# Optimization experiments

Hardware: AMD Instinct MI355X
Metric: run time of the kernel (lower is better)

Reference implementation:

```python
import jax, jax.numpy as jnp
import numpy as np

V, E, H, L, T, B, S = 50000, 256, 512, 2, 22, 64, 512
HH = H // 2
START, STOP = T - 2, T - 1  # START_TAG, STOP_TAG appended to tagset


def _lstm_cell(x, h, c, wih, whh, b):
    # PyTorch gate order: i, f, g, o
    g = x @ wih.T + h @ whh.T + b
    i, f, gg, o = jnp.split(g, 4, axis=-1)
    c2 = jax.nn.sigmoid(f) * c + jax.nn.sigmoid(i) * jnp.tanh(gg)
    h2 = jax.nn.sigmoid(o) * jnp.tanh(c2)
    return h2, c2


def _run_dir(xs, ms, h0, c0, wih, whh, b, reverse):
    # xs: [S,B,E], ms: [S,B] bool. Packed-sequence semantics: no state update
    # and zero (pad-value) output at padded steps.
    def step(carry, inp):
        h, c = carry
        xt, mt = inp
        h2, c2 = _lstm_cell(xt, h, c, wih, whh, b)
        m = mt[:, None]
        h = jnp.where(m, h2, h)
        c = jnp.where(m, c2, c)
        return (h, c), jnp.where(m, h, 0.0)
    _, outs = jax.lax.scan(step, (h0, c0), (xs, ms), reverse=reverse)
    return outs


def _forward_feats(sentence, lengths, emb, wih_f, whh_f, b_f, wih_b, whh_b, b_b,
                   h1_0, c1_0, wih_s, whh_s, b_s, h2_0, c2_0, W_tag, b_tag):
    Bq, Sq = sentence.shape
    x = emb[sentence]                                       # [B,S,E]
    ms = (jnp.arange(Sq)[None, :] < lengths[:, None]).T     # [S,B]
    xs = jnp.transpose(x, (1, 0, 2))                        # [S,B,E]
    bc = lambda p: jnp.broadcast_to(p, (Bq, p.shape[-1]))
    out_f = _run_dir(xs, ms, bc(h1_0[0]), bc(c1_0[0]), wih_f, whh_f, b_f, False)
    out_b = _run_dir(xs, ms, bc(h1_0[1]), bc(c1_0[1]), wih_b, whh_b, b_b, True)
    bi = jnp.concatenate([out_f, out_b], axis=-1)           # [S,B,H]

    h0 = jnp.broadcast_to(h2_0, (L, Bq, H))
    c0 = jnp.broadcast_to(c2_0, (L, Bq, H))

    def step(carry, xt):
        h, c = carry
        inp = xt
        hs, cs = [], []
        for l in range(L):  # small fixed layer count
            h2, c2 = _lstm_cell(inp, h[l], c[l], wih_s[l], whh_s[l], b_s[l])
            inp = h2
            hs.append(h2)
            cs.append(c2)
        return (jnp.stack(hs), jnp.stack(cs)), inp

    _, outs = jax.lax.scan(step, (h0, c0), bi)              # [S,B,H]
    feats = jnp.einsum('sbh,th->sbt', outs, W_tag) + b_tag  # [S,B,T]
    return feats, ms


def _viterbi(feats, ms, trans):
    # trans[i, j] = score of transitioning from tag j to tag i
    Tn = trans.shape[0]
    score = feats[0] + trans[:, START][None, :]             # [B,T]

    def vstep(score, inp):
        ft, mt = inp
        cand = score[:, None, :] + trans[None, :, :]        # [B, to, from]
        ns = jnp.max(cand, axis=2) + ft
        bp = jnp.argmax(cand, axis=2)
        m = mt[:, None]
        score = jnp.where(m, ns, score)
        bp = jnp.where(m, bp, jnp.arange(Tn)[None, :])      # identity at pad
        return score, bp

    score, bps = jax.lax.scan(vstep, score, (feats[1:], ms[1:]))
    terminal = score + trans[STOP][None, :]
    best_score = jnp.max(terminal, axis=1)                  # [B]
    best_tag = jnp.argmax(terminal, axis=1)                 # [B]

    def bt(tag, bp):
        nt = jnp.take_along_axis(bp, tag[:, None], axis=1)[:, 0]
        return nt, nt

    _, rest = jax.lax.scan(bt, best_tag, bps, reverse=True)  # [S-1,B]
    tags = jnp.concatenate([rest, best_tag[None, :]], axis=0).T  # [B,S]
    return best_score, tags


def setup_inputs() -> dict:
    key = jax.random.key(0)
    ks = iter(jax.random.split(key, 24))
    sc = 0.08
    n = lambda shape: jax.random.normal(next(ks), shape, dtype=jnp.float32) * sc
    return dict(
        sentence=jax.random.randint(next(ks), (B, S), 0, V),
        lengths=jax.random.randint(next(ks), (B,), 1, S + 1),
        emb=n((V, E)),
        wih_f=n((4 * HH, E)), whh_f=n((4 * HH, HH)), b_f=n((4 * HH,)),
        wih_b=n((4 * HH, E)), whh_b=n((4 * HH, HH)), b_b=n((4 * HH,)),
        h1_0=n((2, 1, HH)), c1_0=n((2, 1, HH)),
        wih_s=n((L, 4 * H, H)), whh_s=n((L, 4 * H, H)), b_s=n((L, 4 * H)),
        h2_0=n((L, 1, H)), c2_0=n((L, 1, H)),
        W_tag=n((T, H)), b_tag=n((T,)),
        trans=n((T, T)),
    )


def reference(sentence, lengths, emb, wih_f, whh_f, b_f, wih_b, whh_b, b_b,
              h1_0, c1_0, wih_s, whh_s, b_s, h2_0, c2_0, W_tag, b_tag, trans):
    feats, ms = _forward_feats(sentence, lengths, emb, wih_f, whh_f, b_f,
                               wih_b, whh_b, b_b, h1_0, c1_0,
                               wih_s, whh_s, b_s, h2_0, c2_0, W_tag, b_tag)
    score, tag_seq = _viterbi(feats, ms, trans)
    return score, tag_seq
```

## Files before the change

### kernel.cpp

```cpp
#include <hip/hip_runtime.h>
#include <cmath>


namespace {
constexpr int SS = 512;
constexpr int BB = 64;
constexpr int EE = 256;
constexpr int HHd = 256;
constexpr int HD = 512;
constexpr int NTAG = 22;
constexpr int TSTART = 20;
constexpr int TSTOP = 21;

constexpr size_t OFF_BI    = 0;
constexpr size_t OFF_H1H   = OFF_BI    + (size_t)SS * HD * BB;
constexpr size_t OFF_XT    = OFF_H1H   + (size_t)(SS + 1) * HD * BB;
constexpr size_t OFF_FEATS = OFF_XT    + (size_t)SS * EE * BB;
constexpr size_t OFF_H0R   = OFF_FEATS + (size_t)SS * NTAG * BB;
constexpr size_t OFF_HF    = OFF_H0R   + 2 * (size_t)HD * BB;
constexpr size_t OFF_HB    = OFF_HF    + 2 * (size_t)HHd * BB;
constexpr size_t OFF_BAR   = OFF_HB    + 2 * (size_t)HHd * BB;
constexpr int BAR_INTS = 1152;

constexpr size_t OFF_C0 = OFF_XT;
constexpr size_t OFF_C1 = OFF_XT + (size_t)HD * BB;
}

__device__ __forceinline__ int cidx(int k, int lane) {
  return ((k >> 2) << 8) + (lane << 2) + (k & 3);
}

__device__ __forceinline__ float4 cload4(const float4* p) {
  float4 r;
  asm volatile("global_load_dwordx4 %0, %1, off sc0 sc1" : "=v"(r) : "v"(p));
  return r;
}
__device__ __forceinline__ void vwait0() {
  asm volatile("s_waitcnt vmcnt(0)" ::: "memory");
}
__device__ __forceinline__ void cstore(float* p, float v) {
  __hip_atomic_store(p, v, __ATOMIC_RELAXED, __HIP_MEMORY_SCOPE_AGENT);
}

template <int NBLK>
__device__ __forceinline__ void gbarC(int* flags, int* release, int bid, int epoch) {
  __syncthreads();
  if (threadIdx.x == 0) {
    __hip_atomic_store(flags + bid, epoch + 1, __ATOMIC_RELAXED, __HIP_MEMORY_SCOPE_AGENT);
  }
  if (bid == 0) {
    if (threadIdx.x < 64) {
      constexpr int PER = NBLK / 64;
      bool ok;
      do {
        ok = true;
#pragma unroll
        for (int i = 0; i < PER; ++i) {
          ok = ok && (__hip_atomic_load(flags + threadIdx.x * PER + i, __ATOMIC_RELAXED,
                                        __HIP_MEMORY_SCOPE_AGENT) > epoch);
        }
      } while (__any(!ok));
      if (threadIdx.x == 0) {
        __hip_atomic_store(release, epoch + 1, __ATOMIC_RELAXED, __HIP_MEMORY_SCOPE_AGENT);
      }
    }
  } else {
    if (threadIdx.x == 0) {
      while (__hip_atomic_load(release, __ATOMIC_RELAXED, __HIP_MEMORY_SCOPE_AGENT) <= epoch) {
        __builtin_amdgcn_s_sleep(1);
      }
    }
  }
  __syncthreads();
}

__device__ __forceinline__ float sigm(float x) { return 1.f / (1.f + expf(-x)); }
__device__ __forceinline__ float comp4(float4 v, int w) {
  return (w == 0) ? v.x : (w == 1) ? v.y : (w == 2) ? v.z : v.w;
}

__global__ __launch_bounds__(256) void k0(const int* __restrict__ sent,
                                          const float* __restrict__ emb,
                                          float* __restrict__ xT) {
  const int t = blockIdx.x;
  const int lane = threadIdx.x & 63;
  const int w = __builtin_amdgcn_readfirstlane(threadIdx.x >> 6);
  __shared__ float tile[64][65];
  __shared__ int rows[64];
  if (threadIdx.x < 64) rows[threadIdx.x] = sent[(size_t)threadIdx.x * SS + t];
  __syncthreads();
  float4* xT4 = (float4*)xT;
  for (int e0 = 0; e0 < EE; e0 += 64) {
    for (int bb = 0; bb < 16; ++bb) {
      int b = bb * 4 + w;
      tile[b][lane] = emb[(size_t)rows[b] * EE + e0 + lane];
    }
    __syncthreads();
    for (int r = 0; r < 4; ++r) {
      int ecl = w * 4 + r;
      int ec = (e0 >> 2) + ecl;
      float4 v = make_float4(tile[lane][ecl * 4 + 0], tile[lane][ecl * 4 + 1],
                             tile[lane][ecl * 4 + 2], tile[lane][ecl * 4 + 3]);
      xT4[((size_t)t * 64 + ec) * 64 + lane] = v;
    }
    __syncthreads();
  }
}

struct K2A {
  const float* xT; float* bi;
  const float* wih_f; const float* whh_f; const float* b_f;
  const float* wih_b; const float* whh_b; const float* b_b;
  const float* h10; const float* c10; const int* lengths;
  float* hf; float* hb;
  int* bar;
};

__global__ __launch_bounds__(1024, 1) void k2(K2A a) {
  const int lane = threadIdx.x & 63;
  const int w = __builtin_amdgcn_readfirstlane((int)threadIdx.x >> 6);
  const int d = (int)blockIdx.x >> 7;
  const int lb = (int)blockIdx.x & 127;
  int* flags = a.bar + d * 384;
  int* release = a.bar + d * 384 + 160;
  const int u0 = lb * 2;
  const float* wih = d ? a.wih_b : a.wih_f;
  const float* whh = d ? a.whh_b : a.whh_f;
  const float* bias = d ? a.b_b : a.b_f;
  float* hbuf = d ? a.hb : a.hf;

  __shared__ float lw[8 * 512];
  __shared__ float4 part[16][2][64];

  {
    int f4 = (int)threadIdx.x;
    int r = f4 >> 7;
    int kk = (f4 & 127) * 4;
    int g = r >> 1, ul = r & 1;
    int grow = g * HHd + u0 + ul;
    float4 v = (kk < 256) ? *(const float4*)(wih + (size_t)grow * 256 + kk)
                          : *(const float4*)(whh + (size_t)grow * 256 + (kk - 256));
    *(float4*)(lw + r * 512 + kk) = v;
  }

  const int len = a.lengths[lane];
  float c_st = 0.f, h_old = 0.f;
  if (w < 2) {
    int u = u0 + w;
    h_old = a.h10[d * 256 + u];
    c_st = a.c10[d * 256 + u];
    cstore(&hbuf[cidx(u, lane)], h_old);
    vwait0();
  }
  int ep = 0;
  gbarC<128>(flags, release, lb, ep); ep++;

  const int ks = w * 32;
  const bool hpart = (w >= 8);
  const float4* lw4 = (const float4*)lw;
  int buf = 0;
  for (int step = 0; step < SS; ++step) {
    const int t = d ? (SS - 1 - step) : step;
    const float* actbase = hpart ? (hbuf + (size_t)buf * (HHd * 64))
                                 : (a.xT + (size_t)t * (EE * 64));
    const int ksl = hpart ? (ks - 256) : ks;
    const float4* p = (const float4*)actbase + (size_t)(ksl >> 2) * 64 + lane;
    float4 va[8];
    if (hpart) {
#pragma unroll
      for (int c = 0; c < 8; ++c) va[c] = cload4(p + (size_t)c * 64);
      vwait0();
    } else {
#pragma unroll
      for (int c = 0; c < 8; ++c) va[c] = p[(size_t)c * 64];
    }
    float acc[8] = {0, 0, 0, 0, 0, 0, 0, 0};
#pragma unroll
    for (int c = 0; c < 8; ++c) {
      float4 h = va[c];
#pragma unroll
      for (int r = 0; r < 8; ++r) {
        float4 wv = lw4[r * 128 + (ks >> 2) + c];
        acc[r] = fmaf(h.x, wv.x, acc[r]);
        acc[r] = fmaf(h.y, wv.y, acc[r]);
        acc[r] = fmaf(h.z, wv.z, acc[r]);
        acc[r] = fmaf(h.w, wv.w, acc[r]);
      }
    }
    part[w][0][lane] = make_float4(acc[0], acc[1], acc[2], acc[3]);
    part[w][1][lane] = make_float4(acc[4], acc[5], acc[6], acc[7]);
    __syncthreads();
    if (w < 2) {
      float qi = 0.f, qf = 0.f, qg = 0.f, qo = 0.f;
#pragma unroll
      for (int wv = 0; wv < 16; ++wv) {
        float4 p0 = part[wv][0][lane], p1 = part[wv][1][lane];
        qi += comp4(p0, w);  qf += comp4(p0, 2 + w);
        qg += comp4(p1, w);  qo += comp4(p1, 2 + w);
      }
      const int u = u0 + w;
      float gi = qi + bias[u];
      float gf = qf + bias[256 + u];
      float gg = qg + bias[512 + u];
      float go = qo + bias[768 + u];
      float i_ = sigm(gi), f_ = sigm(gf), o_ = sigm(go);
      float gn = tanhf(gg);
      float c2 = f_ * c_st + i_ * gn;
      float h2 = o_ * tanhf(c2);
      const bool m = (t < len);
      h2 = m ? h2 : h_old;
      c_st = m ? c2 : c_st;
      h_old = h2;
      cstore(&hbuf[(size_t)(buf ^ 1) * (HHd * 64) + cidx(u, lane)], h2);
      a.bi[(size_t)t * (HD * 64) + cidx(d * 256 + u, lane)] = m ? h2 : 0.f;
      vwait0();
    }
    buf ^= 1;
    gbarC<128>(flags, release, lb, ep); ep++;
  }
}

__global__ __launch_bounds__(512) void k4i(const float* __restrict__ h20,
                                           const float* __restrict__ c20,
                                           float* __restrict__ h0r,
                                           float* __restrict__ h1h,
                                           float* __restrict__ c0,
                                           float* __restrict__ c1) {
  const int layer = blockIdx.x;
  const int u = threadIdx.x;
  const float hv = h20[layer * 512 + u];
  const float cv = c20[layer * 512 + u];
  float* hd = layer ? h1h : h0r;
  float* cd = layer ? c1 : c0;
#pragma unroll 4
  for (int lane = 0; lane < 64; ++lane) {
    hd[cidx(u, lane)] = hv;
    cd[cidx(u, lane)] = cv;
  }
}

struct K4S {
  const float* bi; float* h0r; float* h1h;
  const float* wihs; const float* whhs; const float* bs;
  float* c0; float* c1;
};

__global__ __launch_bounds__(1024, 1) void k4s(K4S a, int t) {
  const int layer = (int)blockIdx.x >> 7;
  if (layer == 0) { if (t >= SS) return; } else { if (t < 1) return; }
  const int lane = threadIdx.x & 63;
  const int w = __builtin_amdgcn_readfirstlane((int)threadIdx.x >> 6);
  const int lb = (int)blockIdx.x & 127;
  const int u0 = lb * 4;
  const float* wih = a.wihs + (size_t)layer * (2048 * 512);
  const float* whh = a.whhs + (size_t)layer * (2048 * 512);

  __shared__ float part[8][16][64];

  float* cst = layer ? a.c1 : a.c0;
  float c_st = 0.f;
  if (w < 4) c_st = cst[cidx(u0 + w, lane)];

  const int ks = (w & 7) * 64;
  const bool hpart = (w >= 8);
  const float* wsel = hpart ? whh : wih;
  const float* wr[16];
#pragma unroll
  for (int g = 0; g < 4; ++g)
#pragma unroll
    for (int ul = 0; ul < 4; ++ul)
      wr[g * 4 + ul] = wsel + (size_t)(g * HD + u0 + ul) * HD + ks;

  const float* actbase;
  if (layer == 0)
    actbase = hpart ? (a.h0r + (size_t)(t & 1) * (HD * 64))
                    : (a.bi + (size_t)t * (HD * 64));
  else
    actbase = hpart ? (a.h1h + (size_t)(t - 1) * (HD * 64))
                    : (a.h0r + (size_t)(t & 1) * (HD * 64));

  const float4* p = (const float4*)actbase + (size_t)(ks >> 2) * 64 + lane;
  float4 va[16];
#pragma unroll
  for (int c = 0; c < 16; ++c) va[c] = p[(size_t)c * 64];

  float acc[16] = {0, 0, 0, 0, 0, 0, 0, 0, 0, 0, 0, 0, 0, 0, 0, 0};
#pragma unroll
  for (int c = 0; c < 16; ++c) {
    float4 h = va[c];
    const int k = c * 4;
#pragma unroll
    for (int r = 0; r < 16; ++r) {
      float4 wv = *(const float4*)(wr[r] + k);
      acc[r] = fmaf(h.x, wv.x, acc[r]);
      acc[r] = fmaf(h.y, wv.y, acc[r]);
      acc[r] = fmaf(h.z, wv.z, acc[r]);
      acc[r] = fmaf(h.w, wv.w, acc[r]);
    }
  }
  if (w < 8) {
#pragma unroll
    for (int r = 0; r < 16; ++r) part[w][r][lane] = acc[r];
  }
  __syncthreads();
  if (w >= 8) {
#pragma unroll
    for (int r = 0; r < 16; ++r) part[w - 8][r][lane] += acc[r];
  }
  __syncthreads();
  if (w < 4) {
    float q[4];
#pragma unroll
    for (int g = 0; g < 4; ++g) {
      float s = 0.f;
#pragma unroll
      for (int sl = 0; sl < 8; ++sl) s += part[sl][g * 4 + w][lane];
      q[g] = s;
    }
    const int u = u0 + w;
    const float* bsl = a.bs + (size_t)layer * 2048;
    float gi = q[0] + bsl[u];
    float gf = q[1] + bsl[512 + u];
    float gg = q[2] + bsl[1024 + u];
    float go = q[3] + bsl[1536 + u];
    float i_ = sigm(gi), f_ = sigm(gf), o_ = sigm(go);
    float gn = tanhf(gg);
    float c2 = f_ * c_st + i_ * gn;
    float h2 = o_ * tanhf(c2);
    cst[cidx(u, lane)] = c2;
    if (layer == 0)
      a.h0r[(size_t)((t + 1) & 1) * (HD * 64) + cidx(u, lane)] = h2;
    else
      a.h1h[(size_t)t * (HD * 64) + cidx(u, lane)] = h2;
  }
}

__global__ __launch_bounds__(256) void k4b(const float* __restrict__ h1h,
                                           const float* __restrict__ Wtag,
                                           const float* __restrict__ btag,
                                           float* __restrict__ feats) {
  const int t = blockIdx.x;
  const int lane = threadIdx.x & 63;
  const int w = __builtin_amdgcn_readfirstlane(threadIdx.x >> 6);
  const int j0 = w * 6;
  const float4* p = (const float4*)(h1h + (size_t)(t + 1) * (HD * 64)) + lane;
  const float* r[6];
  float acc[6];
#pragma unroll
  for (int jj = 0; jj < 6; ++jj) {
    int j = j0 + jj; if (j > 21) j = 21;
    r[jj] = Wtag + (size_t)j * HD;
    acc[jj] = btag[j];
  }
#pragma unroll 2
  for (int c = 0; c < 128; ++c) {
    float4 h = p[(size_t)c * 64];
    int k = c * 4;
#pragma unroll
    for (int jj = 0; jj < 6; ++jj) {
      acc[jj] = fmaf(h.x, r[jj][k], acc[jj]);
      acc[jj] = fmaf(h.y, r[jj][k + 1], acc[jj]);
      acc[jj] = fmaf(h.z, r[jj][k + 2], acc[jj]);
      acc[jj] = fmaf(h.w, r[jj][k + 3], acc[jj]);
    }
  }
#pragma unroll
  for (int jj = 0; jj < 6; ++jj) {
    int j = j0 + jj;
    if (j < NTAG) feats[((size_t)t * NTAG + j) * 64 + lane] = acc[jj];
  }
}

__global__ __launch_bounds__(64) void k5(const float* __restrict__ feats,
                                         const float* __restrict__ trans,
                                         const int* __restrict__ lengths,
                                         float* __restrict__ out) {
  const int b = blockIdx.x;
  const int j = threadIdx.x;
  __shared__ float tr[NTAG * NTAG];
  __shared__ float sc[NTAG];
  __shared__ float term[NTAG];
  __shared__ unsigned char bp[SS - 1][NTAG];
  for (int i = j; i < NTAG * NTAG; i += 64) tr[i] = trans[i];
  const int len = lengths[b];
  float score = 0.f;
  __syncthreads();
  if (j < NTAG) {
    score = feats[(size_t)j * 64 + b] + tr[j * NTAG + TSTART];
    sc[j] = score;
  }
  __syncthreads();
  for (int t = 1; t < len; ++t) {
    float best = -3.4e38f; int bi_ = 0;
    if (j < NTAG) {
#pragma unroll
      for (int i = 0; i < NTAG; ++i) {
        float c = sc[i] + tr[j * NTAG + i];
        if (c > best) { best = c; bi_ = i; }
      }
      score = best + feats[((size_t)t * NTAG + j) * 64 + b];
      bp[t - 1][j] = (unsigned char)bi_;
    }
    __syncthreads();
    if (j < NTAG) sc[j] = score;
    __syncthreads();
  }
  if (j < NTAG) term[j] = score + tr[TSTOP * NTAG + j];
  __syncthreads();
  if (j == 0) {
    float bs = term[0]; int bt = 0;
    for (int i = 1; i < NTAG; ++i) if (term[i] > bs) { bs = term[i]; bt = i; }
    out[b] = bs;
    int tag = bt;
    for (int t = SS - 1; t >= 1; --t) {
      out[64 + (size_t)b * SS + t] = (float)tag;
      if (t < len) tag = bp[t - 1][tag];
    }
    out[64 + (size_t)b * SS + 0] = (float)tag;
  }
}

extern "C" void kernel_launch(void* const* d_in, const int* in_sizes, int n_in,
                              void* d_out, int out_size, void* d_ws, size_t ws_size,
                              hipStream_t stream) {
  const int* sentence = (const int*)d_in[0];
  const int* lengths  = (const int*)d_in[1];
  const float* emb    = (const float*)d_in[2];
  const float* wih_f  = (const float*)d_in[3];
  const float* whh_f  = (const float*)d_in[4];
  const float* b_f    = (const float*)d_in[5];
  const float* wih_b  = (const float*)d_in[6];
  const float* whh_b  = (const float*)d_in[7];
  const float* b_b    = (const float*)d_in[8];
  const float* h10    = (const float*)d_in[9];
  const float* c10    = (const float*)d_in[10];
  const float* wihs   = (const float*)d_in[11];
  const float* whhs   = (const float*)d_in[12];
  const float* bs     = (const float*)d_in[13];
  const float* h20    = (const float*)d_in[14];
  const float* c20    = (const float*)d_in[15];
  const float* Wtag   = (const float*)d_in[16];
  const float* btag   = (const float*)d_in[17];
  const float* trans  = (const float*)d_in[18];
  float* ws = (float*)d_ws;
  float* out = (float*)d_out;
  int* barbase = (int*)(ws + OFF_BAR);

  hipMemsetAsync((void*)barbase, 0, BAR_INTS * sizeof(int), stream);

  k0<<<dim3(SS), dim3(256), 0, stream>>>(sentence, emb, ws + OFF_XT);

  K2A a2{ws + OFF_XT, ws + OFF_BI, wih_f, whh_f, b_f, wih_b, whh_b, b_b,
         h10, c10, lengths,
         ws + OFF_HF, ws + OFF_HB,
         barbase};
  k2<<<dim3(256), dim3(1024), 0, stream>>>(a2);

  k4i<<<dim3(2), dim3(512), 0, stream>>>(h20, c20, ws + OFF_H0R, ws + OFF_H1H,
                                         ws + OFF_C0, ws + OFF_C1);
  K4S a4{ws + OFF_BI, ws + OFF_H0R, ws + OFF_H1H, wihs, whhs, bs,
         ws + OFF_C0, ws + OFF_C1};
  for (int t = 0; t <= SS; ++t) {
    k4s<<<dim3(256), dim3(1024), 0, stream>>>(a4, t);
  }

  k4b<<<dim3(SS), dim3(256), 0, stream>>>(ws + OFF_H1H, Wtag, btag, ws + OFF_FEATS);
  k5<<<dim3(BB), dim3(64), 0, stream>>>(ws + OFF_FEATS, trans, lengths, out);
}
```

Baseline: 10.46 ms.

## Fold tag projection into per-step stacked LSTM launches with one-step lag

Removes the separate tag-projection kernel and adds an extra block to each per-timestep stacked-LSTM launch that computes feats for the timestep finished two launches earlier. The launch loop gets one extra iteration to drain the last step. The aim is to hide the projection work inside the latency-bound recurrent launches, at the cost of one more launch and an extra block per launch that may lengthen the critical path.

```diff
diff --git a/kernel.cpp b/kernel.cpp
--- a/kernel.cpp
+++ b/kernel.cpp
@@ -243,11 +243,48 @@
   const float* bi; float* h0r; float* h1h;
   const float* wihs; const float* whhs; const float* bs;
   float* c0; float* c1;
+  const float* Wtag; const float* btag; float* feats;
 };
 
 __global__ __launch_bounds__(1024, 1) void k4s(K4S a, int t) {
+  if ((int)blockIdx.x >= 256) {
+    const int tf = t - 2;
+    if (tf < 0 || tf >= SS) return;
+    if ((int)threadIdx.x >= 256) return;
+    const int lane = threadIdx.x & 63;
+    const int w4 = __builtin_amdgcn_readfirstlane((int)threadIdx.x >> 6);
+    const int j0 = w4 * 6;
+    const float4* p = (const float4*)(a.h1h + (size_t)(tf + 1) * (HD * 64)) + lane;
+    const float* r[6];
+    float acc[6];
+#pragma unroll
+    for (int jj = 0; jj < 6; ++jj) {
+      int j = j0 + jj; if (j > 21) j = 21;
+      r[jj] = a.Wtag + (size_t)j * HD;
+      acc[jj] = a.btag[j];
+    }
+#pragma unroll 2
+    for (int c = 0; c < 128; ++c) {
+      float4 h = p[(size_t)c * 64];
+      int k = c * 4;
+#pragma unroll
+      for (int jj = 0; jj < 6; ++jj) {
+        acc[jj] = fmaf(h.x, r[jj][k], acc[jj]);
+        acc[jj] = fmaf(h.y, r[jj][k + 1], acc[jj]);
+        acc[jj] = fmaf(h.z, r[jj][k + 2], acc[jj]);
+        acc[jj] = fmaf(h.w, r[jj][k + 3], acc[jj]);
+      }
+    }
+#pragma unroll
+    for (int jj = 0; jj < 6; ++jj) {
+      int j = j0 + jj;
+      if (j < NTAG) a.feats[((size_t)tf * NTAG + j) * 64 + lane] = acc[jj];
+    }
+    return;
+  }
+
   const int layer = (int)blockIdx.x >> 7;
-  if (layer == 0) { if (t >= SS) return; } else { if (t < 1) return; }
+  if (layer == 0) { if (t >= SS) return; } else { if (t < 1 || t > SS) return; }
   const int lane = threadIdx.x & 63;
   const int w = __builtin_amdgcn_readfirstlane((int)threadIdx.x >> 6);
   const int lb = (int)blockIdx.x & 127;
@@ -332,42 +369,6 @@
       a.h0r[(size_t)((t + 1) & 1) * (HD * 64) + cidx(u, lane)] = h2;
     else
       a.h1h[(size_t)t * (HD * 64) + cidx(u, lane)] = h2;
-  }
-}
-
-__global__ __launch_bounds__(256) void k4b(const float* __restrict__ h1h,
-                                           const float* __restrict__ Wtag,
-                                           const float* __restrict__ btag,
-                                           float* __restrict__ feats) {
-  const int t = blockIdx.x;
-  const int lane = threadIdx.x & 63;
-  const int w = __builtin_amdgcn_readfirstlane(threadIdx.x >> 6);
-  const int j0 = w * 6;
-  const float4* p = (const float4*)(h1h + (size_t)(t + 1) * (HD * 64)) + lane;
-  const float* r[6];
-  float acc[6];
-#pragma unroll
-  for (int jj = 0; jj < 6; ++jj) {
-    int j = j0 + jj; if (j > 21) j = 21;
-    r[jj] = Wtag + (size_t)j * HD;
-    acc[jj] = btag[j];
-  }
-#pragma unroll 2
-  for (int c = 0; c < 128; ++c) {
-    float4 h = p[(size_t)c * 64];
-    int k = c * 4;
-#pragma unroll
-    for (int jj = 0; jj < 6; ++jj) {
-      acc[jj] = fmaf(h.x, r[jj][k], acc[jj]);
-      acc[jj] = fmaf(h.y, r[jj][k + 1], acc[jj]);
-      acc[jj] = fmaf(h.z, r[jj][k + 2], acc[jj]);
-      acc[jj] = fmaf(h.w, r[jj][k + 3], acc[jj]);
-    }
-  }
-#pragma unroll
-  for (int jj = 0; jj < 6; ++jj) {
-    int j = j0 + jj;
-    if (j < NTAG) feats[((size_t)t * NTAG + j) * 64 + lane] = acc[jj];
   }
 }
 
@@ -459,11 +460,11 @@
   k4i<<<dim3(2), dim3(512), 0, stream>>>(h20, c20, ws + OFF_H0R, ws + OFF_H1H,
                                          ws + OFF_C0, ws + OFF_C1);
   K4S a4{ws + OFF_BI, ws + OFF_H0R, ws + OFF_H1H, wihs, whhs, bs,
-         ws + OFF_C0, ws + OFF_C1};
-  for (int t = 0; t <= SS; ++t) {
-    k4s<<<dim3(256), dim3(1024), 0, stream>>>(a4, t);
-  }
-
-  k4b<<<dim3(SS), dim3(256), 0, stream>>>(ws + OFF_H1H, Wtag, btag, ws + OFF_FEATS);
+         ws + OFF_C0, ws + OFF_C1,
+         Wtag, btag, ws + OFF_FEATS};
+  for (int t = 0; t <= SS + 1; ++t) {
+    k4s<<<dim3(257), dim3(1024), 0, stream>>>(a4, t);
+  }
+
   k5<<<dim3(BB), dim3(64), 0, stream>>>(ws + OFF_FEATS, trans, lengths, out);
 }
```

New measurement: 23.38 ms. 123% more time.
